# Performance work log

Measured on AMD Instinct MI355X. Metric: run time of the kernel, lower is better.

The kernel has to match this reference:

```python
import jax, jax.numpy as jnp
import numpy as np

B, S, D = 1, 2048, 4096
H, KV = 32, 8
HD = D // H  # 128
NEG = -1e9


def _rope(t, cos, sin):
    # t: [B,S,h,HD]; cos/sin: [S,HD//2] -> broadcast [1,S,1,HD//2]
    tr = t[..., 0::2]
    ti = t[..., 1::2]
    c = cos[None, :, None, :]
    s = sin[None, :, None, :]
    out_r = tr * c - ti * s
    out_i = tr * s + ti * c
    # interleave back: (..., HD//2, 2) -> (..., HD)
    return jnp.stack([out_r, out_i], axis=-1).reshape(t.shape)


def setup_inputs() -> dict:
    key = jax.random.key(0)
    ks = jax.random.split(key, 5)
    w_scale = 0.02
    x = jax.random.normal(ks[0], (B, S, D), dtype=jnp.float32)
    wq = jax.random.normal(ks[1], (H * HD, D), dtype=jnp.float32) * w_scale
    wk = jax.random.normal(ks[2], (KV * HD, D), dtype=jnp.float32) * w_scale
    wv = jax.random.normal(ks[3], (KV * HD, D), dtype=jnp.float32) * w_scale
    wo = jax.random.normal(ks[4], (D, H * HD), dtype=jnp.float32) * w_scale
    # RoPE tables (theta = 10000)
    inv_freq = 1.0 / (10000.0 ** (np.arange(0, HD, 2, dtype=np.float32) / HD))
    angles = np.arange(S, dtype=np.float32)[:, None] * inv_freq[None, :]  # [S, HD//2]
    freqs_cos = jnp.asarray(np.cos(angles))
    freqs_sin = jnp.asarray(np.sin(angles))
    # causal additive mask [1,1,S,S]
    causal = jnp.tril(jnp.ones((S, S), dtype=bool))
    mask = jnp.where(causal, 0.0, NEG).astype(jnp.float32)[None, None]
    return {"x": x, "wq": wq, "wk": wk, "wv": wv, "wo": wo,
            "freqs_cos": freqs_cos, "freqs_sin": freqs_sin, "mask": mask}


def reference(x, wq, wk, wv, wo, freqs_cos, freqs_sin, mask):
    b, s, d = x.shape
    q = (x @ wq.T).reshape(b, s, H, HD)
    k = (x @ wk.T).reshape(b, s, KV, HD)
    v = (x @ wv.T).reshape(b, s, KV, HD)
    q = _rope(q, freqs_cos, freqs_sin)
    k = _rope(k, freqs_cos, freqs_sin)
    rep = H // KV
    k = jnp.repeat(k, rep, axis=2)  # [b,s,H,HD]
    v = jnp.repeat(v, rep, axis=2)
    scores = jnp.einsum('bshd,bthd->bhst', q, k) / jnp.sqrt(jnp.float32(HD))
    scores = scores + mask
    attn = jax.nn.softmax(scores, axis=-1)
    out = jnp.einsum('bhst,bthd->bshd', attn, v).reshape(b, s, H * HD)
    return out @ wo.T
```

## Files before the change

kernel.cpp:

```cpp
#include <hip/hip_runtime.h>
#include <hip/hip_bf16.h>
#include <math.h>

#define SEQ 2048
#define DIM 4096
#define NH 32
#define NKV 8
#define HD 128
#define KVD 1024
#define SCALE 0.08838834764831845f
#define NEGBIG -1000000000.0f

typedef __bf16 bf16;
typedef __attribute__((ext_vector_type(4))) __bf16 bf16x4;
typedef __attribute__((ext_vector_type(8))) __bf16 bf16x8;
typedef __attribute__((ext_vector_type(4))) float f32x4;

__device__ __forceinline__ void async_g2l16(const bf16* g, bf16* l) {
  __builtin_amdgcn_global_load_lds(
      (const __attribute__((address_space(1))) void*)g,
      (__attribute__((address_space(3))) void*)l,
      16, 0, 0);
}

#define SEG_X  2097152
#define SEG_WQ 4194304
#define SEG_WK 1048576
#define CX0 SEG_X
#define CX1 (CX0 + SEG_WQ)
#define CX2 (CX1 + SEG_WK)
#define CX3 (CX2 + SEG_WK)

__global__ void cast_all_kernel(const float* __restrict__ x,
                                const float* __restrict__ wq,
                                const float* __restrict__ wk,
                                const float* __restrict__ wv,
                                bf16* __restrict__ xb, bf16* __restrict__ wqb,
                                bf16* __restrict__ wkb, bf16* __restrict__ wvb) {
  int i = blockIdx.x * 256 + threadIdx.x;
  const float* src; bf16* dst; int j;
  if (i < CX0)      { src = x;  dst = xb;  j = i; }
  else if (i < CX1) { src = wq; dst = wqb; j = i - CX0; }
  else if (i < CX2) { src = wk; dst = wkb; j = i - CX1; }
  else              { src = wv; dst = wvb; j = i - CX2; }
  float4 v = ((const float4*)src)[j];
  bf16x4 o;
  o[0] = (bf16)v.x; o[1] = (bf16)v.y; o[2] = (bf16)v.z; o[3] = (bf16)v.w;
  ((bf16x4*)dst)[j] = o;
}

#define BAR()       asm volatile("s_barrier" ::: "memory")
#define FENCE4()    asm volatile("s_waitcnt vmcnt(4)" ::: "memory")
#define FENCE_ALL() asm volatile("s_waitcnt vmcnt(0)" ::: "memory")

#define MFMAQ(AH, BC, MO, NO)                                              \
  _Pragma("unroll") for (int m2 = 0; m2 < 4; ++m2)                         \
  _Pragma("unroll") for (int n2 = 0; n2 < 2; ++n2)                         \
  _Pragma("unroll") for (int kk = 0; kk < 2; ++kk)                         \
    acc[(MO) + m2][(NO) + n2] = __builtin_amdgcn_mfma_f32_16x16x32_bf16(   \
        (AH)[m2][kk], (BC)[n2][kk], acc[(MO) + m2][(NO) + n2], 0, 0, 0);

__device__ __forceinline__ void gemm256_core(
    const bf16* __restrict__ Ag,
    const bf16* __restrict__ Bg,
    f32x4 acc[8][4])
{
  __shared__ __align__(16) bf16 As[2 * 256 * 64];
  __shared__ __align__(16) bf16 Bs[2 * 256 * 64];

  const int tid  = threadIdx.x;
  const int lane = tid & 63;
  const int w    = tid >> 6;
  const int l15  = lane & 15;
  const int quad = lane >> 4;
  const int wr2  = (w >> 2) * 128;
  const int wc2  = (w & 3) * 64;

  const int srow = w * 8 + (lane >> 3);
  const int sg8  = ((lane & 7) ^ (lane >> 3)) * 8;
  const bf16* gA = Ag + (size_t)srow * DIM + sg8;
  const bf16* gB = Bg + (size_t)srow * DIM + sg8;
  bf16* lA = As + w * 512;
  bf16* lB = Bs + w * 512;

  const int g0   = (quad ^ (l15 & 7)) * 8;
  const int g1   = g0 ^ 32;
  const int aOff = (wr2 + l15) * 64;
  const int bOff = (wc2 + l15) * 64;

#define STAGE_A(b, kt)                                                     \
  { _Pragma("unroll") for (int hh = 0; hh < 2; ++hh)                       \
    _Pragma("unroll") for (int j = 0; j < 2; ++j)                          \
      async_g2l16(gA + (size_t)(hh * 128 + j * 64) * DIM + (kt) * 64,      \
                  lA + (b) * 16384 + (hh * 128 + j * 64) * 64); }
#define STAGE_B0(b, kt)                                                    \
  { _Pragma("unroll") for (int j = 0; j < 2; ++j)                          \
      async_g2l16(gB + (size_t)(j * 64) * DIM + (kt) * 64,                 \
                  lB + (b) * 16384 + (j * 64) * 64); }
#define STAGE_B1(b, kt)                                                    \
  { _Pragma("unroll") for (int j = 0; j < 2; ++j)                          \
      async_g2l16(gB + (size_t)(128 + j * 64) * DIM + (kt) * 64,           \
                  lB + (b) * 16384 + (128 + j * 64) * 64); }

#define LDA(b, rh, m2, gk) \
  (*(const bf16x8*)(As + (b) * 16384 + aOff + (rh) * 4096 + (m2) * 1024 + (gk)))
#define LDB(b, ch, n2, gk) \
  (*(const bf16x8*)(Bs + (b) * 16384 + bOff + (ch) * 2048 + (n2) * 1024 + (gk)))

  const f32x4 vz = {0.f, 0.f, 0.f, 0.f};
#pragma unroll
  for (int mi = 0; mi < 8; ++mi)
#pragma unroll
    for (int ni = 0; ni < 4; ++ni) acc[mi][ni] = vz;

  STAGE_A(0, 0); STAGE_B0(0, 0); STAGE_B1(0, 0);
  STAGE_B0(1, 1); STAGE_B1(1, 1);
  FENCE4();
  BAR();

  for (int i = 0; i < 32; ++i) {
    const int ktn0 = (2 * i + 2 > 63) ? 63 : 2 * i + 2;
    const int ktn1 = (2 * i + 3 > 63) ? 63 : 2 * i + 3;
    {
      bf16x8 aH[4][2], bC0[2][2], bC1[2][2];
#pragma unroll
      for (int m2 = 0; m2 < 4; ++m2) { aH[m2][0] = LDA(0, 0, m2, g0); aH[m2][1] = LDA(0, 0, m2, g1); }
#pragma unroll
      for (int n2 = 0; n2 < 2; ++n2) { bC0[n2][0] = LDB(0, 0, n2, g0); bC0[n2][1] = LDB(0, 0, n2, g1); }
      STAGE_A(1, 2 * i + 1);
      BAR(); __builtin_amdgcn_s_setprio(1);
      MFMAQ(aH, bC0, 0, 0);
      __builtin_amdgcn_s_setprio(0); BAR();
#pragma unroll
      for (int n2 = 0; n2 < 2; ++n2) { bC1[n2][0] = LDB(0, 1, n2, g0); bC1[n2][1] = LDB(0, 1, n2, g1); }
      BAR(); __builtin_amdgcn_s_setprio(1);
      MFMAQ(aH, bC1, 0, 2);
      __builtin_amdgcn_s_setprio(0); BAR();
#pragma unroll
      for (int m2 = 0; m2 < 4; ++m2) { aH[m2][0] = LDA(0, 1, m2, g0); aH[m2][1] = LDA(0, 1, m2, g1); }
      STAGE_B0(0, ktn0);
      BAR(); __builtin_amdgcn_s_setprio(1);
      MFMAQ(aH, bC1, 4, 2);
      __builtin_amdgcn_s_setprio(0); BAR();
      STAGE_B1(0, ktn0);
      FENCE4();
      BAR(); __builtin_amdgcn_s_setprio(1);
      MFMAQ(aH, bC0, 4, 0);
      __builtin_amdgcn_s_setprio(0); BAR();
    }
    {
      bf16x8 aH[4][2], bC0[2][2], bC1[2][2];
#pragma unroll
      for (int m2 = 0; m2 < 4; ++m2) { aH[m2][0] = LDA(1, 0, m2, g0); aH[m2][1] = LDA(1, 0, m2, g1); }
#pragma unroll
      for (int n2 = 0; n2 < 2; ++n2) { bC0[n2][0] = LDB(1, 0, n2, g0); bC0[n2][1] = LDB(1, 0, n2, g1); }
      STAGE_A(0, ktn0);
      BAR(); __builtin_amdgcn_s_setprio(1);
      MFMAQ(aH, bC0, 0, 0);
      __builtin_amdgcn_s_setprio(0); BAR();
#pragma unroll
      for (int n2 = 0; n2 < 2; ++n2) { bC1[n2][0] = LDB(1, 1, n2, g0); bC1[n2][1] = LDB(1, 1, n2, g1); }
      BAR(); __builtin_amdgcn_s_setprio(1);
      MFMAQ(aH, bC1, 0, 2);
      __builtin_amdgcn_s_setprio(0); BAR();
#pragma unroll
      for (int m2 = 0; m2 < 4; ++m2) { aH[m2][0] = LDA(1, 1, m2, g0); aH[m2][1] = LDA(1, 1, m2, g1); }
      STAGE_B0(1, ktn1);
      BAR(); __builtin_amdgcn_s_setprio(1);
      MFMAQ(aH, bC1, 4, 2);
      __builtin_amdgcn_s_setprio(0); BAR();
      STAGE_B1(1, ktn1);
      FENCE4();
      BAR(); __builtin_amdgcn_s_setprio(1);
      MFMAQ(aH, bC0, 4, 0);
      __builtin_amdgcn_s_setprio(0); BAR();
    }
  }
  FENCE_ALL();
}

__global__ __launch_bounds__(512, 2) void qkv256_kernel(
    const bf16* __restrict__ xb, const bf16* __restrict__ wqb,
    const bf16* __restrict__ wkb, const bf16* __restrict__ wvb,
    const float* __restrict__ wo, bf16* __restrict__ wob,
    const float* __restrict__ fc, const float* __restrict__ fs,
    bf16* __restrict__ Qb, bf16* __restrict__ Kb, bf16* __restrict__ Vt)
{
  const int bid = blockIdx.x;
  const int tid = threadIdx.x;
  if (bid >= 192) {
    for (int j = (bid - 192) * 512 + tid; j < SEG_WQ; j += 64 * 512) {
      float4 v = ((const float4*)wo)[j];
      bf16x4 o;
      o[0] = (bf16)v.x; o[1] = (bf16)v.y; o[2] = (bf16)v.z; o[3] = (bf16)v.w;
      ((bf16x4*)wob)[j] = o;
    }
    return;
  }
  const int mTile = bid & 7;
  const int nTile = bid >> 3;
  const bf16* Bg;
  if (nTile < 16)      Bg = wqb + (size_t)nTile * 256 * DIM;
  else if (nTile < 20) Bg = wkb + (size_t)(nTile - 16) * 256 * DIM;
  else                 Bg = wvb + (size_t)(nTile - 20) * 256 * DIM;

  f32x4 acc[8][4];
  gemm256_core(xb + (size_t)mTile * 256 * DIM, Bg, acc);

  const int lane = tid & 63;
  const int w    = tid >> 6;
  const int l15  = lane & 15;
  const int quad = lane >> 4;
  const int wr2  = (w >> 2) * 128;
  const int wc2  = (w & 3) * 64;
  const int sBase = mTile * 256 + wr2 + quad * 4;
  const int nBase = nTile * 256 + wc2;

  if (nTile < 20) {
    const bool isQ = nTile < 16;
    bf16* dst      = isQ ? Qb : Kb;
    const int ldd  = isQ ? DIM : KVD;
    const float sc = isQ ? SCALE : 1.0f;
    const int cOff = isQ ? nBase : nBase - 4096;
    const int odd  = l15 & 1;
#pragma unroll
    for (int mi = 0; mi < 8; ++mi)
#pragma unroll
      for (int ni = 0; ni < 4; ++ni) {
        const int n    = nBase + ni * 16 + l15;
        const int fidx = (n >> 1) & 63;
        const int col  = cOff + ni * 16 + l15;
#pragma unroll
        for (int r = 0; r < 4; ++r) {
          const int s = sBase + mi * 16 + r;
          float v  = acc[mi][ni][r];
          float pv = __shfl_xor(v, 1, 64);
          float c  = fc[s * 64 + fidx];
          float sn = fs[s * 64 + fidx];
          float o  = odd ? (pv * sn + v * c) : (v * c - pv * sn);
          dst[(size_t)s * ldd + col] = (bf16)(o * sc);
        }
      }
  } else {
    const int vBase = nBase - 5120;
#pragma unroll
    for (int mi = 0; mi < 8; ++mi) {
      const int sb = sBase + mi * 16;
#pragma unroll
      for (int ni = 0; ni < 4; ++ni) {
        const int nv = vBase + ni * 16 + l15;
        const int t = nv >> 7, d = nv & 127;
        bf16x4 pv;
#pragma unroll
        for (int r = 0; r < 4; ++r) pv[r] = (bf16)acc[mi][ni][r];
        *(bf16x4*)(Vt + ((size_t)t * HD + d) * SEQ + sb) = pv;
      }
    }
  }
}

__device__ __forceinline__ void gemm128_core(
    const bf16* __restrict__ A, int lda,
    const bf16* __restrict__ B, int ldb,
    int K, int mBase, f32x4 acc[4][4])
{
  __shared__ __align__(16) bf16 As[128 * 32];
  __shared__ __align__(16) bf16 Bs[128 * 32];

  const int tid  = threadIdx.x;
  const int lane = tid & 63;
  const int w    = tid >> 6;
  const int l15  = lane & 15;
  const int quad = lane >> 4;
  const int wr   = (w >> 1) * 64;
  const int wc   = (w & 1) * 64;

  const int srow = lane >> 2;
  const int kswz = ((lane & 3) ^ ((srow >> 1) & 3)) * 8;
  const bf16* gA0 = A + (size_t)(mBase + w * 16 + srow) * lda + kswz;
  const bf16* gA1 = gA0 + (size_t)64 * lda;
  const bf16* gB0 = B + (size_t)(w * 16 + srow) * ldb + kswz;
  const bf16* gB1 = gB0 + (size_t)64 * ldb;
  bf16* lA0 = As + w * 512;
  bf16* lA1 = As + (w + 4) * 512;
  bf16* lB0 = Bs + w * 512;
  bf16* lB1 = Bs + (w + 4) * 512;

  const f32x4 vzero = {0.f, 0.f, 0.f, 0.f};
#pragma unroll
  for (int mi = 0; mi < 4; ++mi)
#pragma unroll
    for (int ni = 0; ni < 4; ++ni) acc[mi][ni] = vzero;

  const int rsw = ((l15 >> 1) & 3);

  for (int k0 = 0; k0 < K; k0 += 32) {
    __syncthreads();
    async_g2l16(gA0 + k0, lA0);
    async_g2l16(gA1 + k0, lA1);
    async_g2l16(gB0 + k0, lB0);
    async_g2l16(gB1 + k0, lB1);
    __syncthreads();

    bf16x8 a[4], b[4];
#pragma unroll
    for (int mi = 0; mi < 4; ++mi)
      a[mi] = *(const bf16x8*)(As + (wr + mi * 16 + l15) * 32 +
                               ((quad ^ rsw) * 8));
#pragma unroll
    for (int ni = 0; ni < 4; ++ni)
      b[ni] = *(const bf16x8*)(Bs + (wc + ni * 16 + l15) * 32 +
                               ((quad ^ rsw) * 8));
#pragma unroll
    for (int mi = 0; mi < 4; ++mi)
#pragma unroll
      for (int ni = 0; ni < 4; ++ni)
        acc[mi][ni] = __builtin_amdgcn_mfma_f32_16x16x32_bf16(
            a[mi], b[ni], acc[mi][ni], 0, 0, 0);
  }
}

__global__ __launch_bounds__(256, 2) void out_gemm_kernel(
    const bf16* __restrict__ attnb, const bf16* __restrict__ wob,
    float* __restrict__ out)
{
  const int mBase = blockIdx.y * 128;
  f32x4 acc[4][4];
  gemm128_core(attnb, DIM, wob + (size_t)blockIdx.x * 128 * DIM, DIM, DIM,
               mBase, acc);

  const int tid  = threadIdx.x;
  const int lane = tid & 63;
  const int w    = tid >> 6;
  const int l15  = lane & 15;
  const int quad = lane >> 4;
  const int wr   = (w >> 1) * 64;
  const int wc   = (w & 1) * 64;
#pragma unroll
  for (int mi = 0; mi < 4; ++mi) {
    int row = mBase + wr + mi * 16 + quad * 4;
#pragma unroll
    for (int ni = 0; ni < 4; ++ni) {
      int col = blockIdx.x * 128 + wc + ni * 16 + l15;
#pragma unroll
      for (int r = 0; r < 4; ++r)
        out[(size_t)(row + r) * DIM + col] = acc[mi][ni][r];
    }
  }
}

__global__ __launch_bounds__(256, 2) void attn_kernel(
    const bf16* __restrict__ Qb, const bf16* __restrict__ Kb,
    const bf16* __restrict__ Vt, bf16* __restrict__ attnb)
{
  __shared__ __align__(16) bf16 Ks[64 * 128];
  __shared__ __align__(16) bf16 Vs[128 * 64];
  __shared__ __align__(16) bf16 Ps[128 * 64];

  const int b    = blockIdx.x;
  const int half = b >> 8;
  const int r8   = b & 255;
  const int h    = (half << 4) | (r8 >> 4);
  const int qt   = half ? (r8 & 15) : 15 - (r8 & 15);
  const int kvh  = h >> 2;
  const int qbase = qt * 128;

  const int tid  = threadIdx.x;
  const int lane = tid & 63;
  const int w    = tid >> 6;
  const int l15  = lane & 15;
  const int quad = lane >> 4;

  bf16x8 qfrag[2][4];
#pragma unroll
  for (int n = 0; n < 2; ++n) {
    int q = qbase + w * 32 + n * 16 + l15;
#pragma unroll
    for (int ks = 0; ks < 4; ++ks)
      qfrag[n][ks] = *(const bf16x8*)(Qb + (size_t)q * DIM + h * HD +
                                      ks * 32 + quad * 8);
  }

  const f32x4 vzero = {0.f, 0.f, 0.f, 0.f};
  f32x4 oacc[8][2];
#pragma unroll
  for (int dm = 0; dm < 8; ++dm)
#pragma unroll
    for (int n = 0; n < 2; ++n) oacc[dm][n] = vzero;
  float m_run[2] = {-1e30f, -1e30f};
  float l_run[2] = {0.f, 0.f};

  const int nkt = 2 * (qt + 1);
  for (int kt = 0; kt < nkt; ++kt) {
    const int kbase = kt * 64;

    __syncthreads();
#pragma unroll
    for (int t = 0; t < 4; ++t) {
      int kr0 = w * 16 + t * 4;
      int krow = kr0 + (lane >> 4);
      int kg = (lane & 15) ^ (krow & 7);
      async_g2l16(Kb + (size_t)(kbase + krow) * KVD + kvh * HD + kg * 8,
                  Ks + kr0 * 128);
      int vr0 = w * 32 + t * 8;
      int d = vr0 + (lane >> 3);
      int vg = (lane & 7) ^ (d & 7);
      async_g2l16(Vt + ((size_t)kvh * HD + d) * SEQ + kbase + vg * 8,
                  Vs + vr0 * 64);
    }
    __syncthreads();

    f32x4 sacc[4][2];
#pragma unroll
    for (int kg = 0; kg < 4; ++kg)
#pragma unroll
      for (int n = 0; n < 2; ++n) sacc[kg][n] = vzero;
#pragma unroll
    for (int kg = 0; kg < 4; ++kg) {
      bf16x8 kf[4];
#pragma unroll
      for (int ks = 0; ks < 4; ++ks) {
        int row = kg * 16 + l15;
        kf[ks] = *(const bf16x8*)(Ks + row * 128 +
                                  (((ks * 4 + quad) ^ (row & 7)) * 8));
      }
#pragma unroll
      for (int n = 0; n < 2; ++n)
#pragma unroll
        for (int ks = 0; ks < 4; ++ks)
          sacc[kg][n] = __builtin_amdgcn_mfma_f32_16x16x32_bf16(
              kf[ks], qfrag[n][ks], sacc[kg][n], 0, 0, 0);
    }

#pragma unroll
    for (int n = 0; n < 2; ++n) {
      const int qloc = w * 32 + n * 16 + l15;
      const int qglob = qbase + qloc;
      if (kbase + 63 > qbase + w * 32 + n * 16) {
#pragma unroll
        for (int kg = 0; kg < 4; ++kg)
#pragma unroll
          for (int r = 0; r < 4; ++r) {
            int key = kbase + kg * 16 + quad * 4 + r;
            if (key > qglob) sacc[kg][n][r] = NEGBIG;
          }
      }
      float mx = -1e30f;
#pragma unroll
      for (int kg = 0; kg < 4; ++kg)
#pragma unroll
        for (int r = 0; r < 4; ++r) mx = fmaxf(mx, sacc[kg][n][r]);
      mx = fmaxf(mx, __shfl_xor(mx, 16, 64));
      mx = fmaxf(mx, __shfl_xor(mx, 32, 64));
      float mnew = fmaxf(m_run[n], mx);
      float alpha = __expf(m_run[n] - mnew);
      m_run[n] = mnew;
      float rs = 0.f;
#pragma unroll
      for (int kg = 0; kg < 4; ++kg) {
        bf16x4 pk;
#pragma unroll
        for (int r = 0; r < 4; ++r) {
          float p = __expf(sacc[kg][n][r] - mnew);
          rs += p;
          pk[r] = (bf16)p;
        }
        int g16 = (kg * 2 + (quad >> 1)) ^ (qloc & 7);
        *(bf16x4*)(Ps + qloc * 64 + g16 * 8 + (quad & 1) * 4) = pk;
      }
      rs += __shfl_xor(rs, 16, 64);
      rs += __shfl_xor(rs, 32, 64);
      l_run[n] = alpha * l_run[n] + rs;
#pragma unroll
      for (int dm = 0; dm < 8; ++dm)
#pragma unroll
        for (int r = 0; r < 4; ++r) oacc[dm][n][r] *= alpha;
    }

    bf16x8 pf[2][2];
#pragma unroll
    for (int kk = 0; kk < 2; ++kk)
#pragma unroll
      for (int n = 0; n < 2; ++n) {
        int qloc = w * 32 + n * 16 + l15;
        pf[kk][n] = *(const bf16x8*)(Ps + qloc * 64 +
                                     (((kk * 4 + quad) ^ (qloc & 7)) * 8));
      }
#pragma unroll
    for (int dm = 0; dm < 8; ++dm) {
#pragma unroll
      for (int kk = 0; kk < 2; ++kk) {
        int d = dm * 16 + l15;
        bf16x8 vf = *(const bf16x8*)(Vs + d * 64 +
                                     (((kk * 4 + quad) ^ (d & 7)) * 8));
#pragma unroll
        for (int n = 0; n < 2; ++n)
          oacc[dm][n] = __builtin_amdgcn_mfma_f32_16x16x32_bf16(
              vf, pf[kk][n], oacc[dm][n], 0, 0, 0);
      }
    }
  }

#pragma unroll
  for (int n = 0; n < 2; ++n) {
    float inv = 1.0f / l_run[n];
    int q = qbase + w * 32 + n * 16 + l15;
#pragma unroll
    for (int dm = 0; dm < 8; ++dm) {
      bf16x4 ov;
#pragma unroll
      for (int r = 0; r < 4; ++r) ov[r] = (bf16)(oacc[dm][n][r] * inv);
      *(bf16x4*)(attnb + (size_t)q * DIM + h * HD + dm * 16 + quad * 4) = ov;
    }
  }
}

extern "C" void kernel_launch(void* const* d_in, const int* in_sizes, int n_in,
                              void* d_out, int out_size, void* d_ws, size_t ws_size,
                              hipStream_t stream) {
  const float* x  = (const float*)d_in[0];
  const float* wq = (const float*)d_in[1];
  const float* wk = (const float*)d_in[2];
  const float* wv = (const float*)d_in[3];
  const float* wo = (const float*)d_in[4];
  const float* fc = (const float*)d_in[5];
  const float* fs = (const float*)d_in[6];
  float* out = (float*)d_out;

  size_t off = 0;
  char* wsb = (char*)d_ws;
  auto take = [&](size_t bytes) -> void* {
    void* p = wsb + off;
    off += (bytes + 255) & ~(size_t)255;
    return p;
  };
  bf16*  xb    = (bf16*)take((size_t)SEQ * DIM * 2);
  bf16*  wqb   = (bf16*)take((size_t)DIM * DIM * 2);
  bf16*  wkb   = (bf16*)take((size_t)KVD * DIM * 2);
  bf16*  wvb   = (bf16*)take((size_t)KVD * DIM * 2);
  bf16*  wob   = (bf16*)take((size_t)DIM * DIM * 2);
  bf16*  Qb    = (bf16*)take((size_t)SEQ * DIM * 2);
  bf16*  Kb    = (bf16*)take((size_t)SEQ * KVD * 2);
  bf16*  Vt    = (bf16*)take((size_t)NKV * HD * SEQ * 2);
  bf16*  attnb = (bf16*)take((size_t)SEQ * DIM * 2);

  cast_all_kernel<<<CX3 / 256, 256, 0, stream>>>(x, wq, wk, wv,
                                                 xb, wqb, wkb, wvb);

  qkv256_kernel<<<dim3(256), 512, 0, stream>>>(xb, wqb, wkb, wvb, wo, wob,
                                               fc, fs, Qb, Kb, Vt);

  attn_kernel<<<dim3(512), 256, 0, stream>>>(Qb, Kb, Vt, attnb);

  out_gemm_kernel<<<dim3(32, 16), 256, 0, stream>>>(attnb, wob, out);
}
```

Baseline: 462.1 us.

## Split A/B staging into half-tiles and interleave loads finer across MFMA phases

Reworks the 256x256 GEMM core's async global-to-LDS staging so that A and B tiles are loaded in half-tile chunks, with each chunk issued as soon as its LDS region is consumed. B staging now maps waves to column slices so each half matches the columns the MFMA quadrants read. The wait count rises from 4 to 6 outstanding loads, keeping more loads in flight. The intent is to start prefetches earlier and overlap memory traffic better with MFMA work, at the cost of more intricate buffer-hazard ordering.

Measured after the change: 479.5 us. +3.8%, slower.

```diff
diff --git a/kernel.cpp b/kernel.cpp
--- a/kernel.cpp
+++ b/kernel.cpp
@@ -50,7 +50,7 @@
 }
 
 #define BAR()       asm volatile("s_barrier" ::: "memory")
-#define FENCE4()    asm volatile("s_waitcnt vmcnt(4)" ::: "memory")
+#define FENCE6()    asm volatile("s_waitcnt vmcnt(6)" ::: "memory")
 #define FENCE_ALL() asm volatile("s_waitcnt vmcnt(0)" ::: "memory")
 
 #define MFMAQ(AH, BC, MO, NO)                                              \
@@ -76,31 +76,26 @@
   const int wr2  = (w >> 2) * 128;
   const int wc2  = (w & 3) * 64;
 
-  const int srow = w * 8 + (lane >> 3);
   const int sg8  = ((lane & 7) ^ (lane >> 3)) * 8;
-  const bf16* gA = Ag + (size_t)srow * DIM + sg8;
-  const bf16* gB = Bg + (size_t)srow * DIM + sg8;
+  const bf16* gA = Ag + (size_t)(w * 8 + (lane >> 3)) * DIM + sg8;
   bf16* lA = As + w * 512;
-  bf16* lB = Bs + w * 512;
+  const bf16* gBn = Bg + (size_t)((w >> 1) * 64 + (w & 1) * 16 +
+                                  (lane >> 3)) * DIM + sg8;
+  bf16* lBn = Bs + ((w >> 1) * 64 + (w & 1) * 16) * 64;
 
   const int g0   = (quad ^ (l15 & 7)) * 8;
   const int g1   = g0 ^ 32;
   const int aOff = (wr2 + l15) * 64;
   const int bOff = (wc2 + l15) * 64;
 
-#define STAGE_A(b, kt)                                                     \
-  { _Pragma("unroll") for (int hh = 0; hh < 2; ++hh)                       \
-    _Pragma("unroll") for (int j = 0; j < 2; ++j)                          \
-      async_g2l16(gA + (size_t)(hh * 128 + j * 64) * DIM + (kt) * 64,      \
-                  lA + (b) * 16384 + (hh * 128 + j * 64) * 64); }
-#define STAGE_B0(b, kt)                                                    \
+#define ST_A(b, ha, kt)                                                    \
   { _Pragma("unroll") for (int j = 0; j < 2; ++j)                          \
-      async_g2l16(gB + (size_t)(j * 64) * DIM + (kt) * 64,                 \
-                  lB + (b) * 16384 + (j * 64) * 64); }
-#define STAGE_B1(b, kt)                                                    \
+      async_g2l16(gA + (size_t)(j * 128 + (ha) * 64) * DIM + (kt) * 64,    \
+                  lA + (b) * 16384 + (j * 128 + (ha) * 64) * 64); }
+#define ST_B(b, hc, kt)                                                    \
   { _Pragma("unroll") for (int j = 0; j < 2; ++j)                          \
-      async_g2l16(gB + (size_t)(128 + j * 64) * DIM + (kt) * 64,           \
-                  lB + (b) * 16384 + (128 + j * 64) * 64); }
+      async_g2l16(gBn + (size_t)((hc) * 32 + j * 8) * DIM + (kt) * 64,     \
+                  lBn + (b) * 16384 + ((hc) * 32 + j * 8) * 64); }
 
 #define LDA(b, rh, m2, gk) \
   (*(const bf16x8*)(As + (b) * 16384 + aOff + (rh) * 4096 + (m2) * 1024 + (gk)))
@@ -113,68 +108,66 @@
 #pragma unroll
     for (int ni = 0; ni < 4; ++ni) acc[mi][ni] = vz;
 
-  STAGE_A(0, 0); STAGE_B0(0, 0); STAGE_B1(0, 0);
-  STAGE_B0(1, 1); STAGE_B1(1, 1);
-  FENCE4();
+  ST_A(0, 0, 0); ST_B(0, 0, 0); ST_B(0, 1, 0); ST_A(0, 1, 0);
+  ST_A(1, 0, 1); ST_B(1, 0, 1); ST_B(1, 1, 1);
+  FENCE6();
   BAR();
 
   for (int i = 0; i < 32; ++i) {
-    const int ktn0 = (2 * i + 2 > 63) ? 63 : 2 * i + 2;
-    const int ktn1 = (2 * i + 3 > 63) ? 63 : 2 * i + 3;
-    {
-      bf16x8 aH[4][2], bC0[2][2], bC1[2][2];
-#pragma unroll
-      for (int m2 = 0; m2 < 4; ++m2) { aH[m2][0] = LDA(0, 0, m2, g0); aH[m2][1] = LDA(0, 0, m2, g1); }
-#pragma unroll
-      for (int n2 = 0; n2 < 2; ++n2) { bC0[n2][0] = LDB(0, 0, n2, g0); bC0[n2][1] = LDB(0, 0, n2, g1); }
-      STAGE_A(1, 2 * i + 1);
-      BAR(); __builtin_amdgcn_s_setprio(1);
-      MFMAQ(aH, bC0, 0, 0);
-      __builtin_amdgcn_s_setprio(0); BAR();
-#pragma unroll
-      for (int n2 = 0; n2 < 2; ++n2) { bC1[n2][0] = LDB(0, 1, n2, g0); bC1[n2][1] = LDB(0, 1, n2, g1); }
-      BAR(); __builtin_amdgcn_s_setprio(1);
-      MFMAQ(aH, bC1, 0, 2);
-      __builtin_amdgcn_s_setprio(0); BAR();
-#pragma unroll
-      for (int m2 = 0; m2 < 4; ++m2) { aH[m2][0] = LDA(0, 1, m2, g0); aH[m2][1] = LDA(0, 1, m2, g1); }
-      STAGE_B0(0, ktn0);
-      BAR(); __builtin_amdgcn_s_setprio(1);
-      MFMAQ(aH, bC1, 4, 2);
-      __builtin_amdgcn_s_setprio(0); BAR();
-      STAGE_B1(0, ktn0);
-      FENCE4();
-      BAR(); __builtin_amdgcn_s_setprio(1);
-      MFMAQ(aH, bC0, 4, 0);
-      __builtin_amdgcn_s_setprio(0); BAR();
-    }
-    {
-      bf16x8 aH[4][2], bC0[2][2], bC1[2][2];
-#pragma unroll
-      for (int m2 = 0; m2 < 4; ++m2) { aH[m2][0] = LDA(1, 0, m2, g0); aH[m2][1] = LDA(1, 0, m2, g1); }
-#pragma unroll
-      for (int n2 = 0; n2 < 2; ++n2) { bC0[n2][0] = LDB(1, 0, n2, g0); bC0[n2][1] = LDB(1, 0, n2, g1); }
-      STAGE_A(0, ktn0);
-      BAR(); __builtin_amdgcn_s_setprio(1);
-      MFMAQ(aH, bC0, 0, 0);
-      __builtin_amdgcn_s_setprio(0); BAR();
-#pragma unroll
-      for (int n2 = 0; n2 < 2; ++n2) { bC1[n2][0] = LDB(1, 1, n2, g0); bC1[n2][1] = LDB(1, 1, n2, g1); }
-      BAR(); __builtin_amdgcn_s_setprio(1);
-      MFMAQ(aH, bC1, 0, 2);
-      __builtin_amdgcn_s_setprio(0); BAR();
-#pragma unroll
-      for (int m2 = 0; m2 < 4; ++m2) { aH[m2][0] = LDA(1, 1, m2, g0); aH[m2][1] = LDA(1, 1, m2, g1); }
-      STAGE_B0(1, ktn1);
-      BAR(); __builtin_amdgcn_s_setprio(1);
-      MFMAQ(aH, bC1, 4, 2);
-      __builtin_amdgcn_s_setprio(0); BAR();
-      STAGE_B1(1, ktn1);
-      FENCE4();
-      BAR(); __builtin_amdgcn_s_setprio(1);
-      MFMAQ(aH, bC0, 4, 0);
-      __builtin_amdgcn_s_setprio(0); BAR();
-    }
+    const int t1 = 2 * i + 1;
+    const int ta = (2 * i + 2 < 64) ? 2 * i + 2 : 63;
+    const int tb = (2 * i + 3 < 64) ? 2 * i + 3 : 63;
+    bf16x8 aH[4][2], bC0[2][2], bC1[2][2];
+#pragma unroll
+    for (int m2 = 0; m2 < 4; ++m2) { aH[m2][0] = LDA(0, 0, m2, g0); aH[m2][1] = LDA(0, 0, m2, g1); }
+#pragma unroll
+    for (int n2 = 0; n2 < 2; ++n2) { bC0[n2][0] = LDB(0, 0, n2, g0); bC0[n2][1] = LDB(0, 0, n2, g1); }
+    ST_A(1, 1, t1);
+    BAR(); __builtin_amdgcn_s_setprio(1);
+    MFMAQ(aH, bC0, 0, 0);
+    __builtin_amdgcn_s_setprio(0); BAR();
+#pragma unroll
+    for (int n2 = 0; n2 < 2; ++n2) { bC1[n2][0] = LDB(0, 1, n2, g0); bC1[n2][1] = LDB(0, 1, n2, g1); }
+    ST_A(0, 0, ta);
+    BAR(); __builtin_amdgcn_s_setprio(1);
+    MFMAQ(aH, bC1, 0, 2);
+    __builtin_amdgcn_s_setprio(0); BAR();
+#pragma unroll
+    for (int m2 = 0; m2 < 4; ++m2) { aH[m2][0] = LDA(0, 1, m2, g0); aH[m2][1] = LDA(0, 1, m2, g1); }
+    ST_B(0, 0, ta);
+    BAR(); __builtin_amdgcn_s_setprio(1);
+    MFMAQ(aH, bC1, 4, 2);
+    __builtin_amdgcn_s_setprio(0); BAR();
+    ST_B(0, 1, ta);
+    FENCE6();
+    BAR(); __builtin_amdgcn_s_setprio(1);
+    MFMAQ(aH, bC0, 4, 0);
+    __builtin_amdgcn_s_setprio(0); BAR();
+#pragma unroll
+    for (int m2 = 0; m2 < 4; ++m2) { aH[m2][0] = LDA(1, 0, m2, g0); aH[m2][1] = LDA(1, 0, m2, g1); }
+#pragma unroll
+    for (int n2 = 0; n2 < 2; ++n2) { bC0[n2][0] = LDB(1, 0, n2, g0); bC0[n2][1] = LDB(1, 0, n2, g1); }
+    ST_A(0, 1, ta);
+    BAR(); __builtin_amdgcn_s_setprio(1);
+    MFMAQ(aH, bC0, 0, 0);
+    __builtin_amdgcn_s_setprio(0); BAR();
+#pragma unroll
+    for (int n2 = 0; n2 < 2; ++n2) { bC1[n2][0] = LDB(1, 1, n2, g0); bC1[n2][1] = LDB(1, 1, n2, g1); }
+    ST_A(1, 0, tb);
+    BAR(); __builtin_amdgcn_s_setprio(1);
+    MFMAQ(aH, bC1, 0, 2);
+    __builtin_amdgcn_s_setprio(0); BAR();
+#pragma unroll
+    for (int m2 = 0; m2 < 4; ++m2) { aH[m2][0] = LDA(1, 1, m2, g0); aH[m2][1] = LDA(1, 1, m2, g1); }
+    ST_B(1, 0, tb);
+    BAR(); __builtin_amdgcn_s_setprio(1);
+    MFMAQ(aH, bC1, 4, 2);
+    __builtin_amdgcn_s_setprio(0); BAR();
+    ST_B(1, 1, tb);
+    FENCE6();
+    BAR(); __builtin_amdgcn_s_setprio(1);
+    MFMAQ(aH, bC0, 4, 0);
+    __builtin_amdgcn_s_setprio(0); BAR();
   }
   FENCE_ALL();
 }
```
